# Kernel tuning notes

Measured on AMD Instinct MI355X. Metric: run time of the kernel, lower is better.

Reference implementation:

```python
import jax, jax.numpy as jnp
import numpy as np

N_CLASSES = 8  # hardcoded by the (-1, 8, 8) reshape in the original layer

def setup_inputs() -> dict:
    key = jax.random.key(0)
    k1, k2, k3, k4 = jax.random.split(key, 4)
    B, F, C, R = 16384, 128, N_CLASSES, 64
    x = jax.random.normal(k1, (B, F), dtype=jnp.float32)
    p = jax.random.uniform(k2, (B, C), dtype=jnp.float32)  # class-prob-like input
    W = jax.random.normal(k3, (F, C * C, R), dtype=jnp.float32) * 0.02
    b = jax.random.normal(k4, (C, C, R), dtype=jnp.float32) * 0.1
    return {"x": x, "p": p, "W": W, "b": b}

def reference(x, p, W, b):
    # x: (B, 128) features; p: (B, C) class probs; W: (128, C*C, R); b: (C, C, R)
    B = x.shape[0]
    C = b.shape[0]
    R = b.shape[-1]
    # per-annotator GEMM fused across all annotators: (B, C*C, R)
    logits = jnp.einsum('bf,fkr->bkr', x, W).reshape(B, C, C, R) + b[None]
    # row-softmax: softmax over the "predicted class" axis for each true class c
    M = jax.nn.softmax(logits, axis=2)  # (B, C, C, R)
    # batched dot: p (B,C) contracted against rows of each annotator matrix
    out = jnp.einsum('bc,bcdr->bdr', p, M)  # (B, C, R)
    # NOTE: original applies K.dropout(0.5) (training-mode); omitted for a
    # deterministic inference reference (identity at eval).
    return out
```

## Files before the change

kernel.cpp:

```cpp
#include <hip/hip_runtime.h>
#include <hip/hip_bf16.h>


#define B_ROWS   16384
#define F_DIM    128
#define NCOL     4096
#define OUT_STRIDE 512
#define LOG2E    1.44269504088896340736f

typedef __bf16 bf16x8 __attribute__((ext_vector_type(8)));
typedef float  f32x4  __attribute__((ext_vector_type(4)));

#define AS1(p) ((const __attribute__((address_space(1))) unsigned int*)(p))
#define AS3(p) ((__attribute__((address_space(3))) unsigned int*)(p))

__global__ void wconv_kernel(const float* __restrict__ W, __bf16* __restrict__ wf) {
    int f    = blockIdx.x * 256 + threadIdx.x;
    int lane = f & 63;
    int tkk  = f >> 6;
    int t    = tkk >> 2;
    int kk   = tkk & 3;
    int kbase = kk * 32 + (lane >> 4) * 8;
    int n     = t * 16 + (lane & 15);
    bf16x8 frag;
    for (int j = 0; j < 8; ++j)
        frag[j] = (__bf16)W[(kbase + j) * NCOL + n];
    *(bf16x8*)(wf + f * 8) = frag;
}

__global__ __launch_bounds__(256, 4)
void fused_kernel(const float* __restrict__ x, const float* __restrict__ p,
                  const float* __restrict__ bias, const __bf16* __restrict__ wf,
                  float* __restrict__ out) {
    __shared__ __align__(16) char lds[32768];

    const int lane = threadIdx.x & 63;
    const int ww   = threadIdx.x >> 6;
    const int quad = lane >> 4;
    const int l15  = lane & 15;
    const int w    = blockIdx.x & 3;
    const int b0   = (blockIdx.x >> 2) * 64 + ww * 16;

    bf16x8 afr[4];
    {
        const float* xr = x + (b0 + l15) * F_DIM + quad * 8;
#pragma unroll
        for (int kk = 0; kk < 4; ++kk) {
            float4 lo = *(const float4*)(xr + kk * 32);
            float4 hi = *(const float4*)(xr + kk * 32 + 4);
            bf16x8 f;
            f[0] = (__bf16)lo.x; f[1] = (__bf16)lo.y;
            f[2] = (__bf16)lo.z; f[3] = (__bf16)lo.w;
            f[4] = (__bf16)hi.x; f[5] = (__bf16)hi.y;
            f[6] = (__bf16)hi.z; f[7] = (__bf16)hi.w;
            afr[kk] = f;
        }
    }

    float O[8][4] = {};

#pragma unroll 1
    for (int c = 0; c < 8; ++c) {
        {
#pragma unroll
            for (int j = 0; j < 8; ++j) {
                int d  = ww * 2 + (j >> 2);
                int kk = j & 3;
                int gf = ((c * 8 + d) * 4 + w) * 4 + kk;
                __builtin_amdgcn_global_load_lds(
                    AS1(wf + (size_t)gf * 512 + lane * 8),
                    AS3(lds + (d * 4 + kk) * 1024), 16, 0, 0);
            }
        }
        __syncthreads();

        float pvv[4];
#pragma unroll
        for (int jj = 0; jj < 4; ++jj)
            pvv[jj] = p[(b0 + quad * 4 + jj) * 8 + c];

        float bvl[8];
#pragma unroll
        for (int d = 0; d < 8; ++d)
            bvl[d] = bias[(c * 8 + d) * 64 + w * 16 + l15] * LOG2E;

        f32x4 acc[8] = {};
#pragma unroll
        for (int kk = 0; kk < 4; ++kk)
#pragma unroll
            for (int d = 0; d < 8; ++d) {
                bf16x8 bfr = *(const bf16x8*)(lds + (d * 4 + kk) * 1024 + lane * 16);
                acc[d] = __builtin_amdgcn_mfma_f32_16x16x32_bf16(
                             afr[kk], bfr, acc[d], 0, 0, 0);
            }

#pragma unroll
        for (int jj = 0; jj < 4; ++jj) {
            float e[8];
#pragma unroll
            for (int d = 0; d < 8; ++d)
                e[d] = __builtin_amdgcn_exp2f(
                           __builtin_fmaf(acc[d][jj], LOG2E, bvl[d]));
            float s01 = e[0] + e[1], s23 = e[2] + e[3];
            float s45 = e[4] + e[5], s67 = e[6] + e[7];
            float s = (s01 + s23) + (s45 + s67);
            float scale = pvv[jj] * __builtin_amdgcn_rcpf(s);
#pragma unroll
            for (int d = 0; d < 8; ++d)
                O[d][jj] = __builtin_fmaf(e[d], scale, O[d][jj]);
        }
        __syncthreads();
    }

#pragma unroll
    for (int jj = 0; jj < 4; ++jj) {
        float* orow = out + (b0 + quad * 4 + jj) * OUT_STRIDE + w * 16 + l15;
#pragma unroll
        for (int d = 0; d < 8; ++d)
            orow[d * 64] = O[d][jj];
    }
}

extern "C" void kernel_launch(void* const* d_in, const int* in_sizes, int n_in,
                              void* d_out, int out_size, void* d_ws, size_t ws_size,
                              hipStream_t stream) {
    const float* x    = (const float*)d_in[0];
    const float* p    = (const float*)d_in[1];
    const float* W    = (const float*)d_in[2];
    const float* bias = (const float*)d_in[3];
    float* out = (float*)d_out;
    __bf16* wf = (__bf16*)d_ws;

    wconv_kernel<<<dim3(256), dim3(256), 0, stream>>>(W, wf);
    fused_kernel<<<dim3(1024), dim3(256), 0, stream>>>(x, p, bias, wf, out);
}
```

Before: 104.2 us.

## Retile fused kernel to 32 rows per wave and split columns eightfold

The weight fragment layout is reorganised so that each MFMA 16-column tile holds two d-values of 8 r each. Each wave now computes 32 batch rows against 4 tiles, reusing each LDS B fragment across two A fragments. The block covers 128 rows and 8 r-slices, which halves LDS per block. The softmax sum over the 8 classes is now completed with a cross-lane shuffle. This raises MFMA work per LDS load and per weight byte, at the cost of more registers (occupancy hint lowered to 3) and an extra shuffle.

```diff
diff --git a/kernel.cpp b/kernel.cpp
--- a/kernel.cpp
+++ b/kernel.cpp
@@ -17,33 +17,40 @@
 __global__ void wconv_kernel(const float* __restrict__ W, __bf16* __restrict__ wf) {
     int f    = blockIdx.x * 256 + threadIdx.x;
     int lane = f & 63;
-    int tkk  = f >> 6;
-    int t    = tkk >> 2;
-    int kk   = tkk & 3;
+    int gf   = f >> 6;
+    int kk   = gf & 3;
+    int w    = (gf >> 2) & 7;
+    int t    = (gf >> 5) & 3;
+    int c    = gf >> 7;
+    int l15  = lane & 15;
     int kbase = kk * 32 + (lane >> 4) * 8;
-    int n     = t * 16 + (lane & 15);
+    int col   = c * 512 + (2 * t + (l15 >> 3)) * 64 + w * 8 + (l15 & 7);
     bf16x8 frag;
+#pragma unroll
     for (int j = 0; j < 8; ++j)
-        frag[j] = (__bf16)W[(kbase + j) * NCOL + n];
-    *(bf16x8*)(wf + f * 8) = frag;
+        frag[j] = (__bf16)W[(kbase + j) * NCOL + col];
+    *(bf16x8*)(wf + (size_t)f * 8) = frag;
 }
 
-__global__ __launch_bounds__(256, 4)
+__global__ __launch_bounds__(256, 3)
 void fused_kernel(const float* __restrict__ x, const float* __restrict__ p,
                   const float* __restrict__ bias, const __bf16* __restrict__ wf,
                   float* __restrict__ out) {
-    __shared__ __align__(16) char lds[32768];
+    __shared__ __align__(16) char lds[16384];
 
     const int lane = threadIdx.x & 63;
     const int ww   = threadIdx.x >> 6;
     const int quad = lane >> 4;
     const int l15  = lane & 15;
-    const int w    = blockIdx.x & 3;
-    const int b0   = (blockIdx.x >> 2) * 64 + ww * 16;
+    const int h    = l15 >> 3;
+    const int q    = l15 & 7;
+    const int w    = blockIdx.x & 7;
+    const int b0   = (blockIdx.x >> 3) * 128 + ww * 32;
 
-    bf16x8 afr[4];
-    {
-        const float* xr = x + (b0 + l15) * F_DIM + quad * 8;
+    bf16x8 afr[2][4];
+#pragma unroll
+    for (int m = 0; m < 2; ++m) {
+        const float* xr = x + (size_t)(b0 + m * 16 + l15) * F_DIM + quad * 8;
 #pragma unroll
         for (int kk = 0; kk < 4; ++kk) {
             float4 lo = *(const float4*)(xr + kk * 32);
@@ -53,72 +60,76 @@
             f[2] = (__bf16)lo.z; f[3] = (__bf16)lo.w;
             f[4] = (__bf16)hi.x; f[5] = (__bf16)hi.y;
             f[6] = (__bf16)hi.z; f[7] = (__bf16)hi.w;
-            afr[kk] = f;
+            afr[m][kk] = f;
         }
     }
 
-    float O[8][4] = {};
+    float O[2][4][4] = {};
 
 #pragma unroll 1
     for (int c = 0; c < 8; ++c) {
         {
+            const __bf16* src = wf + (size_t)(((c * 4 + ww) * 8 + w) * 4) * 512;
 #pragma unroll
-            for (int j = 0; j < 8; ++j) {
-                int d  = ww * 2 + (j >> 2);
-                int kk = j & 3;
-                int gf = ((c * 8 + d) * 4 + w) * 4 + kk;
+            for (int kk = 0; kk < 4; ++kk)
                 __builtin_amdgcn_global_load_lds(
-                    AS1(wf + (size_t)gf * 512 + lane * 8),
-                    AS3(lds + (d * 4 + kk) * 1024), 16, 0, 0);
-            }
+                    AS1(src + kk * 512 + lane * 8),
+                    AS3(lds + (ww * 4 + kk) * 1024), 16, 0, 0);
         }
         __syncthreads();
 
-        float pvv[4];
+        float bvl[4];
 #pragma unroll
-        for (int jj = 0; jj < 4; ++jj)
-            pvv[jj] = p[(b0 + quad * 4 + jj) * 8 + c];
+        for (int t = 0; t < 4; ++t)
+            bvl[t] = bias[c * 512 + (2 * t + h) * 64 + w * 8 + q] * LOG2E;
 
-        float bvl[8];
-#pragma unroll
-        for (int d = 0; d < 8; ++d)
-            bvl[d] = bias[(c * 8 + d) * 64 + w * 16 + l15] * LOG2E;
-
-        f32x4 acc[8] = {};
+        f32x4 acc[2][4] = {};
 #pragma unroll
         for (int kk = 0; kk < 4; ++kk)
 #pragma unroll
-            for (int d = 0; d < 8; ++d) {
-                bf16x8 bfr = *(const bf16x8*)(lds + (d * 4 + kk) * 1024 + lane * 16);
-                acc[d] = __builtin_amdgcn_mfma_f32_16x16x32_bf16(
-                             afr[kk], bfr, acc[d], 0, 0, 0);
+            for (int t = 0; t < 4; ++t) {
+                bf16x8 bfr = *(const bf16x8*)(lds + (t * 4 + kk) * 1024 + lane * 16);
+                acc[0][t] = __builtin_amdgcn_mfma_f32_16x16x32_bf16(
+                                afr[0][kk], bfr, acc[0][t], 0, 0, 0);
+                acc[1][t] = __builtin_amdgcn_mfma_f32_16x16x32_bf16(
+                                afr[1][kk], bfr, acc[1][t], 0, 0, 0);
             }
 
 #pragma unroll
-        for (int jj = 0; jj < 4; ++jj) {
-            float e[8];
+        for (int m = 0; m < 2; ++m) {
 #pragma unroll
-            for (int d = 0; d < 8; ++d)
-                e[d] = __builtin_amdgcn_exp2f(
-                           __builtin_fmaf(acc[d][jj], LOG2E, bvl[d]));
-            float s01 = e[0] + e[1], s23 = e[2] + e[3];
-            float s45 = e[4] + e[5], s67 = e[6] + e[7];
-            float s = (s01 + s23) + (s45 + s67);
-            float scale = pvv[jj] * __builtin_amdgcn_rcpf(s);
-#pragma unroll
-            for (int d = 0; d < 8; ++d)
-                O[d][jj] = __builtin_fmaf(e[d], scale, O[d][jj]);
+            for (int jj = 0; jj < 4; ++jj) {
+                float pv = p[(size_t)(b0 + m * 16 + quad * 4 + jj) * 8 + c];
+                float e0 = __builtin_amdgcn_exp2f(
+                               __builtin_fmaf(acc[m][0][jj], LOG2E, bvl[0]));
+                float e1 = __builtin_amdgcn_exp2f(
+                               __builtin_fmaf(acc[m][1][jj], LOG2E, bvl[1]));
+                float e2 = __builtin_amdgcn_exp2f(
+                               __builtin_fmaf(acc[m][2][jj], LOG2E, bvl[2]));
+                float e3 = __builtin_amdgcn_exp2f(
+                               __builtin_fmaf(acc[m][3][jj], LOG2E, bvl[3]));
+                float s4 = (e0 + e1) + (e2 + e3);
+                float s8 = s4 + __shfl_xor(s4, 8, 64);
+                float scale = pv * __builtin_amdgcn_rcpf(s8);
+                O[m][0][jj] = __builtin_fmaf(e0, scale, O[m][0][jj]);
+                O[m][1][jj] = __builtin_fmaf(e1, scale, O[m][1][jj]);
+                O[m][2][jj] = __builtin_fmaf(e2, scale, O[m][2][jj]);
+                O[m][3][jj] = __builtin_fmaf(e3, scale, O[m][3][jj]);
+            }
         }
         __syncthreads();
     }
 
 #pragma unroll
-    for (int jj = 0; jj < 4; ++jj) {
-        float* orow = out + (b0 + quad * 4 + jj) * OUT_STRIDE + w * 16 + l15;
+    for (int m = 0; m < 2; ++m)
 #pragma unroll
-        for (int d = 0; d < 8; ++d)
-            orow[d * 64] = O[d][jj];
-    }
+        for (int jj = 0; jj < 4; ++jj) {
+            float* orow = out + (size_t)(b0 + m * 16 + quad * 4 + jj) * OUT_STRIDE
+                          + h * 64 + w * 8 + q;
+#pragma unroll
+            for (int t = 0; t < 4; ++t)
+                orow[t * 128] = O[m][t][jj];
+        }
 }
 
 extern "C" void kernel_launch(void* const* d_in, const int* in_sizes, int n_in,
```

Result: slower. 125.3 us (+20.2%).

## Load W fragments directly from global into registers, drop LDS staging and barriers

Applied to the files above, without the earlier changes.

Removes the LDS staging of pre-swizzled bf16 W fragments and the two __syncthreads per class iteration; each wave now loads its B fragments straight from global memory into registers. The block-to-work mapping is changed so blocks sharing the same W column slice (w) are adjacent in launch order, improving L2 reuse of W. The bias is folded into the MFMA accumulator initialisation instead of a separate fma before exp2. The trade-off is that the four waves of a block now each fetch their own W fragments (more global/L2 traffic, higher register pressure) instead of cooperatively sharing them through LDS.

```diff
diff --git a/kernel.cpp b/kernel.cpp
--- a/kernel.cpp
+++ b/kernel.cpp
@@ -11,9 +11,6 @@
 typedef __bf16 bf16x8 __attribute__((ext_vector_type(8)));
 typedef float  f32x4  __attribute__((ext_vector_type(4)));
 
-#define AS1(p) ((const __attribute__((address_space(1))) unsigned int*)(p))
-#define AS3(p) ((__attribute__((address_space(3))) unsigned int*)(p))
-
 __global__ void wconv_kernel(const float* __restrict__ W, __bf16* __restrict__ wf) {
     int f    = blockIdx.x * 256 + threadIdx.x;
     int lane = f & 63;
@@ -23,27 +20,27 @@
     int kbase = kk * 32 + (lane >> 4) * 8;
     int n     = t * 16 + (lane & 15);
     bf16x8 frag;
+#pragma unroll
     for (int j = 0; j < 8; ++j)
         frag[j] = (__bf16)W[(kbase + j) * NCOL + n];
-    *(bf16x8*)(wf + f * 8) = frag;
+    *(bf16x8*)(wf + (size_t)f * 8) = frag;
 }
 
 __global__ __launch_bounds__(256, 4)
 void fused_kernel(const float* __restrict__ x, const float* __restrict__ p,
                   const float* __restrict__ bias, const __bf16* __restrict__ wf,
                   float* __restrict__ out) {
-    __shared__ __align__(16) char lds[32768];
-
     const int lane = threadIdx.x & 63;
     const int ww   = threadIdx.x >> 6;
     const int quad = lane >> 4;
     const int l15  = lane & 15;
-    const int w    = blockIdx.x & 3;
-    const int b0   = (blockIdx.x >> 2) * 64 + ww * 16;
+    const int w    = blockIdx.x >> 8;
+    const int g    = blockIdx.x & 255;
+    const int b0   = g * 64 + ww * 16;
 
     bf16x8 afr[4];
     {
-        const float* xr = x + (b0 + l15) * F_DIM + quad * 8;
+        const float* xr = x + (size_t)(b0 + l15) * F_DIM + quad * 8;
 #pragma unroll
         for (int kk = 0; kk < 4; ++kk) {
             float4 lo = *(const float4*)(xr + kk * 32);
@@ -61,46 +58,42 @@
 
 #pragma unroll 1
     for (int c = 0; c < 8; ++c) {
-        {
-#pragma unroll
-            for (int j = 0; j < 8; ++j) {
-                int d  = ww * 2 + (j >> 2);
-                int kk = j & 3;
-                int gf = ((c * 8 + d) * 4 + w) * 4 + kk;
-                __builtin_amdgcn_global_load_lds(
-                    AS1(wf + (size_t)gf * 512 + lane * 8),
-                    AS3(lds + (d * 4 + kk) * 1024), 16, 0, 0);
-            }
-        }
-        __syncthreads();
-
         float pvv[4];
 #pragma unroll
         for (int jj = 0; jj < 4; ++jj)
-            pvv[jj] = p[(b0 + quad * 4 + jj) * 8 + c];
+            pvv[jj] = p[(size_t)(b0 + quad * 4 + jj) * 8 + c];
 
         float bvl[8];
 #pragma unroll
         for (int d = 0; d < 8; ++d)
-            bvl[d] = bias[(c * 8 + d) * 64 + w * 16 + l15] * LOG2E;
+            bvl[d] = bias[(c * 8 + d) * 64 + w * 16 + l15];
 
-        f32x4 acc[8] = {};
+        f32x4 acc[8];
 #pragma unroll
-        for (int kk = 0; kk < 4; ++kk)
+        for (int d = 0; d < 8; ++d) {
+            f32x4 binit = {bvl[d], bvl[d], bvl[d], bvl[d]};
+            acc[d] = binit;
+        }
+
+        const __bf16* wc = wf + ((size_t)(c * 128 + w * 4)) * 512 + lane * 8;
 #pragma unroll
-            for (int d = 0; d < 8; ++d) {
-                bf16x8 bfr = *(const bf16x8*)(lds + (d * 4 + kk) * 1024 + lane * 16);
+        for (int kk = 0; kk < 4; ++kk) {
+            bf16x8 bfr[8];
+#pragma unroll
+            for (int d = 0; d < 8; ++d)
+                bfr[d] = *(const bf16x8*)(wc + (size_t)(d * 16 + kk) * 512);
+#pragma unroll
+            for (int d = 0; d < 8; ++d)
                 acc[d] = __builtin_amdgcn_mfma_f32_16x16x32_bf16(
-                             afr[kk], bfr, acc[d], 0, 0, 0);
-            }
+                             afr[kk], bfr[d], acc[d], 0, 0, 0);
+        }
 
 #pragma unroll
         for (int jj = 0; jj < 4; ++jj) {
             float e[8];
 #pragma unroll
             for (int d = 0; d < 8; ++d)
-                e[d] = __builtin_amdgcn_exp2f(
-                           __builtin_fmaf(acc[d][jj], LOG2E, bvl[d]));
+                e[d] = __builtin_amdgcn_exp2f(acc[d][jj] * LOG2E);
             float s01 = e[0] + e[1], s23 = e[2] + e[3];
             float s45 = e[4] + e[5], s67 = e[6] + e[7];
             float s = (s01 + s23) + (s45 + s67);
@@ -109,12 +102,11 @@
             for (int d = 0; d < 8; ++d)
                 O[d][jj] = __builtin_fmaf(e[d], scale, O[d][jj]);
         }
-        __syncthreads();
     }
 
 #pragma unroll
     for (int jj = 0; jj < 4; ++jj) {
-        float* orow = out + (b0 + quad * 4 + jj) * OUT_STRIDE + w * 16 + l15;
+        float* orow = out + (size_t)(b0 + quad * 4 + jj) * OUT_STRIDE + w * 16 + l15;
 #pragma unroll
         for (int d = 0; d < 8; ++d)
             orow[d * 64] = O[d][jj];
```

Result: slower. 139.4 us (+33.8%).
